# Optimization experiments

Hardware: AMD Instinct MI355X
Metric: run time of the kernel (lower is better)

## Reference

```python
import jax, jax.numpy as jnp
import numpy as np

B, S, D = 8, 1024, 512
H, Q, V = 8, 64, 64
NEG_INF = -2.0**32 + 1.0  # faithful to the TF module's mask fill value


def setup_inputs() -> dict:
    key = jax.random.key(0)
    ks = jax.random.split(key, 9)
    s = lambda fan_in: 1.0 / np.sqrt(fan_in)
    return {
        "x": jax.random.normal(ks[0], (B, S, D), dtype=jnp.float32),
        "Wq": jax.random.normal(ks[1], (D, Q * H), dtype=jnp.float32) * s(D),
        "bq": jnp.zeros((Q * H,), dtype=jnp.float32),
        "Wk": jax.random.normal(ks[2], (D, Q * H), dtype=jnp.float32) * s(D),
        "bk": jnp.zeros((Q * H,), dtype=jnp.float32),
        "Wv": jax.random.normal(ks[3], (D, V * H), dtype=jnp.float32) * s(D),
        "bv": jnp.zeros((V * H,), dtype=jnp.float32),
        "Wo": jax.random.normal(ks[4], (V * H, D), dtype=jnp.float32) * s(V * H),
        "bo": jnp.zeros((D,), dtype=jnp.float32),
    }


def _split_heads(t, hd):
    # [B,S,h*hd] -> split along last axis into h, concat along axis0 -> [h*B,S,hd]
    b, seq, _ = t.shape
    return t.reshape(b, seq, H, hd).transpose(2, 0, 1, 3).reshape(H * b, seq, hd)


def reference(x, Wq, bq, Wk, bk, Wv, bv, Wo, bo):
    q = _split_heads(x @ Wq + bq, Q)  # [h*B, S, q]
    k = _split_heads(x @ Wk + bk, Q)  # [h*B, S, q]
    v = _split_heads(x @ Wv + bv, V)  # [h*B, S, v]

    score = jnp.einsum("nsq,ntq->nst", q, k)  # [h*B, S, S], NOTE: no 1/sqrt(d) scaling (faithful)
    heatmap_score = score

    # stage == 'train': causal mask, masked entries set to -2^32 + 1
    mask = jnp.tril(jnp.ones((S, S), dtype=bool))
    score = jnp.where(mask, score, jnp.full_like(score, NEG_INF))
    attn = jax.nn.softmax(score, axis=-1)

    wv = jnp.einsum("nst,ntv->nsv", attn, v)  # [h*B, S, v]
    # split along axis0 into h, concat along last axis -> [B, S, h*v]
    wv = wv.reshape(H, B, S, V).transpose(1, 2, 0, 3).reshape(B, S, H * V)
    out = wv @ Wo + bo  # [B, S, D]
    return (out, heatmap_score)
```

## Files before the change

### kernel.cpp

```cpp
#include <hip/hip_runtime.h>


typedef unsigned short u16;
typedef unsigned int u32;
typedef __attribute__((ext_vector_type(8))) short bf8;
typedef __attribute__((ext_vector_type(4))) float f4;

__device__ __forceinline__ u16 f2bf(float f) {
    u32 x = __builtin_bit_cast(u32, f);
    return (u16)((x + 0x7FFFu + ((x >> 16) & 1u)) >> 16);
}

#define MFMA16(a, b, c) __builtin_amdgcn_mfma_f32_16x16x32_bf16((a), (b), (c), 0, 0, 0)

#define GLD16(gp, lp) __builtin_amdgcn_global_load_lds( \
    (const __attribute__((address_space(1))) unsigned int*)(gp), \
    (__attribute__((address_space(3))) unsigned int*)(lp), 16, 0, 0)

__global__ __launch_bounds__(256) void k_cvt_x(const float4* __restrict__ xi,
                                               ushort4* __restrict__ xo)
{
    int idx = blockIdx.x * 256 + threadIdx.x;
    for (int i = idx; i < 1048576; i += 262144) {
        float4 f = xi[i];
        ushort4 o;
        o.x = f2bf(f.x); o.y = f2bf(f.y); o.z = f2bf(f.z); o.w = f2bf(f.w);
        xo[i] = o;
    }
}

__global__ __launch_bounds__(256) void k_cvt_wT(
    const float* __restrict__ Wq, const float* __restrict__ Wk,
    const float* __restrict__ Wv, const float* __restrict__ Wo,
    u16* __restrict__ WqT, u16* __restrict__ WkT,
    u16* __restrict__ WvT, u16* __restrict__ WoT)
{
    const int z = blockIdx.z;
    const float* __restrict__ W = (z == 0) ? Wq : (z == 1) ? Wk : (z == 2) ? Wv : Wo;
    u16* __restrict__ WT        = (z == 0) ? WqT : (z == 1) ? WkT : (z == 2) ? WvT : WoT;

    __shared__ __align__(16) u16 Ts[64 * 72];
    const int k0 = blockIdx.x * 64, c0 = blockIdx.y * 64;
    const int tid = threadIdx.x;
    const int r = tid >> 4, cc = (tid & 15) * 4;
    #pragma unroll
    for (int rr = r; rr < 64; rr += 16) {
        float4 f = *(const float4*)&W[(size_t)(k0 + rr) * 512 + c0 + cc];
        Ts[(cc + 0) * 72 + rr] = f2bf(f.x);
        Ts[(cc + 1) * 72 + rr] = f2bf(f.y);
        Ts[(cc + 2) * 72 + rr] = f2bf(f.z);
        Ts[(cc + 3) * 72 + rr] = f2bf(f.w);
    }
    __syncthreads();
    #pragma unroll
    for (int i = 0; i < 2; ++i) {
        int gi = tid + i * 256;
        int cr = gi >> 3, g = gi & 7;
        bf8 v = *(bf8*)&Ts[cr * 72 + g * 8];
        *(bf8*)&WT[(size_t)(c0 + cr) * 512 + k0 + g * 8] = v;
    }
}

__global__ __launch_bounds__(256) void k_qkv(
    const u16* __restrict__ xb,
    const u16* __restrict__ WqT, const u16* __restrict__ WkT, const u16* __restrict__ WvT,
    const float* __restrict__ bq, const float* __restrict__ bk, const float* __restrict__ bv,
    u16* __restrict__ qb, u16* __restrict__ kb, u16* __restrict__ vT)
{
    const int which = blockIdx.z;
    const u16* __restrict__ WT     = (which == 0) ? WqT : (which == 1) ? WkT : WvT;
    const float* __restrict__ bias = (which == 0) ? bq : (which == 1) ? bk : bv;

    const int colTile = blockIdx.x * 128;
    const int rowTile = blockIdx.y * 128;

    __shared__ __align__(16) u16 As[128 * 64];
    __shared__ __align__(16) u16 Bs[128 * 64];

    const int tid = threadIdx.x;
    const int lane = tid & 63, w = tid >> 6;
    const int lm = lane & 15, kq = lane >> 4;
    const int mB = (w >> 1) * 64, nB = (w & 1) * 64;

    const int sr = lane >> 3;
    const int sg = (lane & 7) ^ sr;

    f4 acc[4][4] = {};

    for (int k0 = 0; k0 < 512; k0 += 64) {
        __syncthreads();
        #pragma unroll
        for (int i = 0; i < 4; ++i) {
            const int rb = w * 32 + i * 8;
            GLD16(&xb[(size_t)(rowTile + rb + sr) * 512 + k0 + sg * 8], &As[rb * 64]);
            GLD16(&WT[(size_t)(colTile + rb + sr) * 512 + k0 + sg * 8], &Bs[rb * 64]);
        }
        __syncthreads();
        #pragma unroll
        for (int ks = 0; ks < 2; ++ks) {
            bf8 a[4], b[4];
            #pragma unroll
            for (int mi = 0; mi < 4; ++mi)
                a[mi] = *(bf8*)&As[(mB + mi * 16 + lm) * 64 + (((ks * 4 + kq) ^ (lm & 7)) * 8)];
            #pragma unroll
            for (int ni = 0; ni < 4; ++ni)
                b[ni] = *(bf8*)&Bs[(nB + ni * 16 + lm) * 64 + (((ks * 4 + kq) ^ (lm & 7)) * 8)];
            #pragma unroll
            for (int mi = 0; mi < 4; ++mi)
                #pragma unroll
                for (int ni = 0; ni < 4; ++ni)
                    acc[mi][ni] = MFMA16(a[mi], b[ni], acc[mi][ni]);
        }
    }

    if (which < 2) {
        u16* __restrict__ outp = (which == 0) ? qb : kb;
        #pragma unroll
        for (int mi = 0; mi < 4; ++mi) {
            const int r0 = rowTile + mB + mi * 16 + kq * 4;
            #pragma unroll
            for (int ni = 0; ni < 4; ++ni) {
                const int c = colTile + nB + ni * 16 + lm;
                const float bv_ = bias[c];
                const int h = c >> 6, hd = c & 63;
                #pragma unroll
                for (int rg = 0; rg < 4; ++rg) {
                    const int rr = r0 + rg;
                    const int b = rr >> 10, s = rr & 1023;
                    outp[(size_t)(((h * 8 + b) << 10) + s) * 64 + hd] = f2bf(acc[mi][ni][rg] + bv_);
                }
            }
        }
    } else {
        #pragma unroll
        for (int mi = 0; mi < 4; ++mi) {
            const int r0 = rowTile + mB + mi * 16 + kq * 4;
            const int b = r0 >> 10, s0 = r0 & 1023;
            #pragma unroll
            for (int ni = 0; ni < 4; ++ni) {
                const int c = colTile + nB + ni * 16 + lm;
                const float bv_ = bias[c];
                const int h = c >> 6, hd = c & 63;
                ushort4 pk;
                pk.x = f2bf(acc[mi][ni][0] + bv_);
                pk.y = f2bf(acc[mi][ni][1] + bv_);
                pk.z = f2bf(acc[mi][ni][2] + bv_);
                pk.w = f2bf(acc[mi][ni][3] + bv_);
                *(ushort4*)&vT[(size_t)((h * 8 + b) * 64 + hd) * 1024 + s0] = pk;
            }
        }
    }
}

__global__ __launch_bounds__(256) void k_attn(
    const u16* __restrict__ qb, const u16* __restrict__ kb, const u16* __restrict__ vT,
    float* __restrict__ heat, u16* __restrict__ wvb)
{
    const int bid = blockIdx.x;
    const int sT = (bid < 256) ? (7 - (bid >> 6)) : ((bid >> 6) - 4);
    const int n = bid & 63;
    const int s0 = sT * 128;

    __shared__ __align__(16) u16 Kb[2][128 * 64];
    __shared__ __align__(16) u16 Vb[2][64 * 128];

    const int tid = threadIdx.x;
    const int lane = tid & 63, w = tid >> 6;
    const int lm = lane & 15, kq = lane >> 4;
    const int mB = w * 32;

    const int sr = lane >> 3, sg = (lane & 7) ^ sr;
    const int vr = lane >> 4, vg = lane & 15;

    const u16* __restrict__ qn = qb + (size_t)n * 65536;
    const u16* __restrict__ kn = kb + (size_t)n * 65536;
    const u16* __restrict__ vn = vT + (size_t)n * 65536;
    float* __restrict__ hp = heat + ((size_t)n << 20);

    #pragma unroll
    for (int i = 0; i < 4; ++i) {
        const int rb = w * 32 + i * 8;
        GLD16(&kn[(size_t)(rb + sr) * 64 + sg * 8], &Kb[0][rb * 64]);
    }
    #pragma unroll
    for (int i = 0; i < 4; ++i) {
        const int rb = w * 16 + i * 4;
        const int r = rb + vr;
        GLD16(&vn[(size_t)r * 1024 + ((vg ^ (r & 7)) * 8)], &Vb[0][rb * 128]);
    }

    bf8 aq[2][2];
    #pragma unroll
    for (int mi = 0; mi < 2; ++mi)
        #pragma unroll
        for (int ks = 0; ks < 2; ++ks)
            aq[mi][ks] = *(const bf8*)&qn[(size_t)(s0 + mB + mi * 16 + lm) * 64 + ks * 32 + kq * 8];

    f4 accO[2][4] = {};
    float m_i[2][4], l_i[2][4];
    #pragma unroll
    for (int mi = 0; mi < 2; ++mi)
        #pragma unroll
        for (int rg = 0; rg < 4; ++rg) { m_i[mi][rg] = -3.0e38f; l_i[mi][rg] = 0.f; }

    int c = 0;
    for (int tt = 0; tt < 8; ++tt, c ^= 1) {
        const int t0 = tt * 128;
        const bool causal = (tt <= sT);
        u16* __restrict__ Kc = &Kb[c][0];
        u16* __restrict__ Vc = &Vb[c][0];

        __syncthreads();

        if (tt < 7) {
            u16* __restrict__ Kn2 = &Kb[c ^ 1][0];
            #pragma unroll
            for (int i = 0; i < 4; ++i) {
                const int rb = w * 32 + i * 8;
                GLD16(&kn[(size_t)(t0 + 128 + rb + sr) * 64 + sg * 8], &Kn2[rb * 64]);
            }
            if (tt + 1 <= sT) {
                u16* __restrict__ Vn2 = &Vb[c ^ 1][0];
                #pragma unroll
                for (int i = 0; i < 4; ++i) {
                    const int rb = w * 16 + i * 4;
                    const int r = rb + vr;
                    GLD16(&vn[(size_t)r * 1024 + t0 + 128 + ((vg ^ (r & 7)) * 8)], &Vn2[rb * 128]);
                }
            }
        }

        f4 accS[2][8] = {};
        __builtin_amdgcn_s_setprio(1);
        #pragma unroll
        for (int ks = 0; ks < 2; ++ks) {
            bf8 b[8];
            #pragma unroll
            for (int ni = 0; ni < 8; ++ni)
                b[ni] = *(bf8*)&Kc[(ni * 16 + lm) * 64 + (((ks * 4 + kq) ^ (lm & 7)) * 8)];
            #pragma unroll
            for (int mi = 0; mi < 2; ++mi)
                #pragma unroll
                for (int ni = 0; ni < 8; ++ni)
                    accS[mi][ni] = MFMA16(aq[mi][ks], b[ni], accS[mi][ni]);
        }
        __builtin_amdgcn_s_setprio(0);

        #pragma unroll
        for (int mi = 0; mi < 2; ++mi) {
            #pragma unroll
            for (int rg = 0; rg < 4; ++rg) {
                float* rowp = &hp[(size_t)(s0 + mB + mi * 16 + kq * 4 + rg) * 1024 + t0 + lm];
                #pragma unroll
                for (int ni = 0; ni < 8; ++ni)
                    __builtin_nontemporal_store(accS[mi][ni][rg], &rowp[ni * 16]);
            }
        }

        if (causal) {
            asm volatile("s_waitcnt lgkmcnt(0)" ::: "memory");
            __builtin_amdgcn_s_barrier();
            __builtin_amdgcn_sched_barrier(0);

            const bool diag = (tt == sT);
            #pragma unroll
            for (int mi = 0; mi < 2; ++mi) {
                #pragma unroll
                for (int rg = 0; rg < 4; ++rg) {
                    const int srow = s0 + mB + mi * 16 + kq * 4 + rg;
                    float tm = -3.0e38f;
                    #pragma unroll
                    for (int ni = 0; ni < 8; ++ni) {
                        float sv = accS[mi][ni][rg];
                        if (diag && (t0 + ni * 16 + lm > srow)) sv = -3.0e38f;
                        tm = fmaxf(tm, sv);
                    }
                    tm = fmaxf(tm, __shfl_xor(tm, 1));
                    tm = fmaxf(tm, __shfl_xor(tm, 2));
                    tm = fmaxf(tm, __shfl_xor(tm, 4));
                    tm = fmaxf(tm, __shfl_xor(tm, 8));
                    const float mn = fmaxf(m_i[mi][rg], tm);
                    const float alpha = __expf(m_i[mi][rg] - mn);
                    float rs = 0.f;
                    #pragma unroll
                    for (int ni = 0; ni < 8; ++ni) {
                        float sv = accS[mi][ni][rg];
                        const bool ok = !diag || (t0 + ni * 16 + lm <= srow);
                        float p = ok ? __expf(sv - mn) : 0.f;
                        rs += p;
                        accS[mi][ni][rg] = p;
                    }
                    rs += __shfl_xor(rs, 1);
                    rs += __shfl_xor(rs, 2);
                    rs += __shfl_xor(rs, 4);
                    rs += __shfl_xor(rs, 8);
                    l_i[mi][rg] = l_i[mi][rg] * alpha + rs;
                    m_i[mi][rg] = mn;
                    #pragma unroll
                    for (int vni = 0; vni < 4; ++vni) accO[mi][vni][rg] *= alpha;
                }
            }

            #pragma unroll
            for (int half = 0; half < 2; ++half) {
                #pragma unroll
                for (int mi = 0; mi < 2; ++mi) {
                    #pragma unroll
                    for (int rg = 0; rg < 4; ++rg) {
                        const int prow = mB + mi * 16 + kq * 4 + rg;
                        #pragma unroll
                        for (int nl = 0; nl < 4; ++nl) {
                            const float p = accS[mi][half * 4 + nl][rg];
                            Kc[prow * 64 + (((nl * 2 + (lm >> 3)) ^ (prow & 7)) * 8) + (lm & 7)] = f2bf(p);
                        }
                    }
                }
                asm volatile("s_waitcnt lgkmcnt(0)" ::: "memory");
                __builtin_amdgcn_sched_barrier(0);

                __builtin_amdgcn_s_setprio(1);
                #pragma unroll
                for (int kl = 0; kl < 2; ++kl) {
                    const int ks = half * 2 + kl;
                    bf8 a[2], b[4];
                    #pragma unroll
                    for (int mi = 0; mi < 2; ++mi)
                        a[mi] = *(bf8*)&Kc[(mB + mi * 16 + lm) * 64 + (((kl * 4 + kq) ^ (lm & 7)) * 8)];
                    #pragma unroll
                    for (int vni = 0; vni < 4; ++vni)
                        b[vni] = *(bf8*)&Vc[(vni * 16 + lm) * 128 + (((ks * 4 + kq) ^ (lm & 7)) * 8)];
                    #pragma unroll
                    for (int mi = 0; mi < 2; ++mi)
                        #pragma unroll
                        for (int vni = 0; vni < 4; ++vni)
                            accO[mi][vni] = MFMA16(a[mi], b[vni], accO[mi][vni]);
                }
                __builtin_amdgcn_s_setprio(0);

                if (half == 0) {
                    asm volatile("s_waitcnt lgkmcnt(0)" ::: "memory");
                    __builtin_amdgcn_sched_barrier(0);
                }
            }
        }
    }

    u16* __restrict__ wn = wvb + (size_t)n * 65536;
    #pragma unroll
    for (int mi = 0; mi < 2; ++mi) {
        #pragma unroll
        for (int rg = 0; rg < 4; ++rg) {
            const float li = 1.0f / l_i[mi][rg];
            const int s = s0 + mB + mi * 16 + kq * 4 + rg;
            #pragma unroll
            for (int vni = 0; vni < 4; ++vni)
                wn[(size_t)s * 64 + vni * 16 + lm] = f2bf(accO[mi][vni][rg] * li);
        }
    }
}

__global__ __launch_bounds__(256) void k_out(
    const u16* __restrict__ wvb, const u16* __restrict__ WoT, const float* __restrict__ bo,
    float* __restrict__ outp)
{
    const int colTile = blockIdx.x * 128;
    const int rowTile = blockIdx.y * 128;
    const int b = rowTile >> 10, s0 = rowTile & 1023;

    __shared__ __align__(16) u16 As[128 * 64];
    __shared__ __align__(16) u16 Bs[128 * 64];

    const int tid = threadIdx.x;
    const int lane = tid & 63, w = tid >> 6;
    const int lm = lane & 15, kq = lane >> 4;
    const int mB = (w >> 1) * 64, nB = (w & 1) * 64;

    const int sr = lane >> 3;
    const int sg = (lane & 7) ^ sr;

    f4 acc[4][4] = {};

    for (int k0 = 0; k0 < 512; k0 += 64) {
        const int h = k0 >> 6;
        const u16* __restrict__ abase = wvb + (size_t)((h * 8 + b) * 1024 + s0) * 64;
        __syncthreads();
        #pragma unroll
        for (int i = 0; i < 4; ++i) {
            const int rb = w * 32 + i * 8;
            GLD16(&abase[(size_t)(rb + sr) * 64 + sg * 8], &As[rb * 64]);
            GLD16(&WoT[(size_t)(colTile + rb + sr) * 512 + k0 + sg * 8], &Bs[rb * 64]);
        }
        __syncthreads();
        #pragma unroll
        for (int ks = 0; ks < 2; ++ks) {
            bf8 a[4], b2[4];
            #pragma unroll
            for (int mi = 0; mi < 4; ++mi)
                a[mi] = *(bf8*)&As[(mB + mi * 16 + lm) * 64 + (((ks * 4 + kq) ^ (lm & 7)) * 8)];
            #pragma unroll
            for (int ni = 0; ni < 4; ++ni)
                b2[ni] = *(bf8*)&Bs[(nB + ni * 16 + lm) * 64 + (((ks * 4 + kq) ^ (lm & 7)) * 8)];
            #pragma unroll
            for (int mi = 0; mi < 4; ++mi)
                #pragma unroll
                for (int ni = 0; ni < 4; ++ni)
                    acc[mi][ni] = MFMA16(a[mi], b2[ni], acc[mi][ni]);
        }
    }

    #pragma unroll
    for (int mi = 0; mi < 4; ++mi) {
        const int r0 = rowTile + mB + mi * 16 + kq * 4;
        #pragma unroll
        for (int ni = 0; ni < 4; ++ni) {
            const int c = colTile + nB + ni * 16 + lm;
            const float bv_ = bo[c];
            #pragma unroll
            for (int rg = 0; rg < 4; ++rg)
                __builtin_nontemporal_store(acc[mi][ni][rg] + bv_,
                                            &outp[(size_t)(r0 + rg) * 512 + c]);
        }
    }
}

extern "C" void kernel_launch(void* const* d_in, const int* in_sizes, int n_in,
                              void* d_out, int out_size, void* d_ws, size_t ws_size,
                              hipStream_t stream)
{
    (void)in_sizes; (void)n_in; (void)out_size; (void)ws_size;

    const float* x  = (const float*)d_in[0];
    const float* Wq = (const float*)d_in[1];
    const float* bq = (const float*)d_in[2];
    const float* Wk = (const float*)d_in[3];
    const float* bk = (const float*)d_in[4];
    const float* Wv = (const float*)d_in[5];
    const float* bv = (const float*)d_in[6];
    const float* Wo = (const float*)d_in[7];
    const float* bo = (const float*)d_in[8];

    float* outp = (float*)d_out;
    float* heat = outp + 4194304;

    u16* ws16 = (u16*)d_ws;
    u16* xb  = ws16;
    u16* WqT = xb  + 4194304;
    u16* WkT = WqT + 262144;
    u16* WvT = WkT + 262144;
    u16* WoT = WvT + 262144;
    u16* qb  = WoT + 262144;
    u16* kb  = qb  + 4194304;
    u16* vT  = kb  + 4194304;
    u16* wvb = vT  + 4194304;

    k_cvt_x <<<1024, 256, 0, stream>>>((const float4*)x, (ushort4*)xb);
    k_cvt_wT<<<dim3(8, 8, 4), 256, 0, stream>>>(Wq, Wk, Wv, Wo, WqT, WkT, WvT, WoT);
    k_qkv   <<<dim3(4, 64, 3), 256, 0, stream>>>(xb, WqT, WkT, WvT, bq, bk, bv, qb, kb, vT);
    k_attn  <<<dim3(512), 256, 0, stream>>>(qb, kb, vT, heat, wvb);
    k_out   <<<dim3(4, 64), 256, 0, stream>>>(wvb, WoT, bo, outp);
}
```

Baseline: 389.1 us.

## Halve attention query tile to 64 rows, single-buffer V, remap blocks

Each attention block now handles 64 query rows (16 per wave) instead of 128, so the grid doubles to 1024 blocks with launch bounds requesting 3 blocks per SM. V is single-buffered and loaded within the current iteration, guarded by a vmcnt wait, which cuts LDS use. Block-to-head/row-tile mapping is reordered to interleave heads and balance causal work. The aim is more parallelism and occupancy for the heatmap-write-bound kernel, at the cost of reloading K for twice as many blocks and exposing V load latency.

```diff
diff --git a/kernel.cpp b/kernel.cpp
--- a/kernel.cpp
+++ b/kernel.cpp
@@ -152,22 +152,26 @@
     }
 }
 
-__global__ __launch_bounds__(256) void k_attn(
+__global__ __launch_bounds__(256, 3) void k_attn(
     const u16* __restrict__ qb, const u16* __restrict__ kb, const u16* __restrict__ vT,
     float* __restrict__ heat, u16* __restrict__ wvb)
 {
     const int bid = blockIdx.x;
-    const int sT = (bid < 256) ? (7 - (bid >> 6)) : ((bid >> 6) - 4);
-    const int n = bid & 63;
-    const int s0 = sT * 128;
+    const int p = bid >> 3;
+    const int n = (bid & 7) * 8 + (p & 7);
+    const int i4 = p >> 3;
+    const int q2 = i4 >> 2, j4 = i4 & 3;
+    const int rT = (q2 == 0) ? 15 - j4 : (q2 == 1) ? 8 + j4 : (q2 == 2) ? 7 - j4 : j4;
+    const int s0 = rT * 64;
+    const int sTT = rT >> 1;
 
     __shared__ __align__(16) u16 Kb[2][128 * 64];
-    __shared__ __align__(16) u16 Vb[2][64 * 128];
+    __shared__ __align__(16) u16 Vs[64 * 128];
 
     const int tid = threadIdx.x;
     const int lane = tid & 63, w = tid >> 6;
     const int lm = lane & 15, kq = lane >> 4;
-    const int mB = w * 32;
+    const int mB = w * 16;
 
     const int sr = lane >> 3, sg = (lane & 7) ^ sr;
     const int vr = lane >> 4, vg = lane & 15;
@@ -178,59 +182,47 @@
     float* __restrict__ hp = heat + ((size_t)n << 20);
 
     #pragma unroll
-    for (int i = 0; i < 4; ++i) {
-        const int rb = w * 32 + i * 8;
+    for (int ii = 0; ii < 4; ++ii) {
+        const int rb = w * 32 + ii * 8;
         GLD16(&kn[(size_t)(rb + sr) * 64 + sg * 8], &Kb[0][rb * 64]);
     }
-    #pragma unroll
-    for (int i = 0; i < 4; ++i) {
-        const int rb = w * 16 + i * 4;
-        const int r = rb + vr;
-        GLD16(&vn[(size_t)r * 1024 + ((vg ^ (r & 7)) * 8)], &Vb[0][rb * 128]);
-    }
-
-    bf8 aq[2][2];
-    #pragma unroll
-    for (int mi = 0; mi < 2; ++mi)
-        #pragma unroll
-        for (int ks = 0; ks < 2; ++ks)
-            aq[mi][ks] = *(const bf8*)&qn[(size_t)(s0 + mB + mi * 16 + lm) * 64 + ks * 32 + kq * 8];
-
-    f4 accO[2][4] = {};
-    float m_i[2][4], l_i[2][4];
-    #pragma unroll
-    for (int mi = 0; mi < 2; ++mi)
-        #pragma unroll
-        for (int rg = 0; rg < 4; ++rg) { m_i[mi][rg] = -3.0e38f; l_i[mi][rg] = 0.f; }
+
+    bf8 aq[2];
+    #pragma unroll
+    for (int ks = 0; ks < 2; ++ks)
+        aq[ks] = *(const bf8*)&qn[(size_t)(s0 + mB + lm) * 64 + ks * 32 + kq * 8];
+
+    f4 accO[4] = {};
+    float m_i[4], l_i[4];
+    #pragma unroll
+    for (int rg = 0; rg < 4; ++rg) { m_i[rg] = -3.0e38f; l_i[rg] = 0.f; }
 
     int c = 0;
     for (int tt = 0; tt < 8; ++tt, c ^= 1) {
         const int t0 = tt * 128;
-        const bool causal = (tt <= sT);
+        const bool causal = (tt <= sTT);
         u16* __restrict__ Kc = &Kb[c][0];
-        u16* __restrict__ Vc = &Vb[c][0];
 
         __syncthreads();
 
+        if (causal) {
+            #pragma unroll
+            for (int ii = 0; ii < 4; ++ii) {
+                const int rb = w * 16 + ii * 4;
+                const int r = rb + vr;
+                GLD16(&vn[(size_t)r * 1024 + t0 + ((vg ^ (r & 7)) * 8)], &Vs[rb * 128]);
+            }
+        }
         if (tt < 7) {
             u16* __restrict__ Kn2 = &Kb[c ^ 1][0];
             #pragma unroll
-            for (int i = 0; i < 4; ++i) {
-                const int rb = w * 32 + i * 8;
+            for (int ii = 0; ii < 4; ++ii) {
+                const int rb = w * 32 + ii * 8;
                 GLD16(&kn[(size_t)(t0 + 128 + rb + sr) * 64 + sg * 8], &Kn2[rb * 64]);
             }
-            if (tt + 1 <= sT) {
-                u16* __restrict__ Vn2 = &Vb[c ^ 1][0];
-                #pragma unroll
-                for (int i = 0; i < 4; ++i) {
-                    const int rb = w * 16 + i * 4;
-                    const int r = rb + vr;
-                    GLD16(&vn[(size_t)r * 1024 + t0 + 128 + ((vg ^ (r & 7)) * 8)], &Vn2[rb * 128]);
-                }
-            }
-        }
-
-        f4 accS[2][8] = {};
+        }
+
+        f4 accS[8] = {};
         __builtin_amdgcn_s_setprio(1);
         #pragma unroll
         for (int ks = 0; ks < 2; ++ks) {
@@ -239,80 +231,69 @@
             for (int ni = 0; ni < 8; ++ni)
                 b[ni] = *(bf8*)&Kc[(ni * 16 + lm) * 64 + (((ks * 4 + kq) ^ (lm & 7)) * 8)];
             #pragma unroll
-            for (int mi = 0; mi < 2; ++mi)
-                #pragma unroll
-                for (int ni = 0; ni < 8; ++ni)
-                    accS[mi][ni] = MFMA16(aq[mi][ks], b[ni], accS[mi][ni]);
+            for (int ni = 0; ni < 8; ++ni)
+                accS[ni] = MFMA16(aq[ks], b[ni], accS[ni]);
         }
         __builtin_amdgcn_s_setprio(0);
 
         #pragma unroll
-        for (int mi = 0; mi < 2; ++mi) {
-            #pragma unroll
-            for (int rg = 0; rg < 4; ++rg) {
-                float* rowp = &hp[(size_t)(s0 + mB + mi * 16 + kq * 4 + rg) * 1024 + t0 + lm];
-                #pragma unroll
-                for (int ni = 0; ni < 8; ++ni)
-                    __builtin_nontemporal_store(accS[mi][ni][rg], &rowp[ni * 16]);
-            }
+        for (int rg = 0; rg < 4; ++rg) {
+            float* rowp = &hp[(size_t)(s0 + mB + kq * 4 + rg) * 1024 + t0 + lm];
+            #pragma unroll
+            for (int ni = 0; ni < 8; ++ni)
+                __builtin_nontemporal_store(accS[ni][rg], &rowp[ni * 16]);
         }
 
         if (causal) {
-            asm volatile("s_waitcnt lgkmcnt(0)" ::: "memory");
+            asm volatile("s_waitcnt vmcnt(0) lgkmcnt(0)" ::: "memory");
             __builtin_amdgcn_s_barrier();
             __builtin_amdgcn_sched_barrier(0);
 
-            const bool diag = (tt == sT);
-            #pragma unroll
-            for (int mi = 0; mi < 2; ++mi) {
+            const bool diag = (tt == sTT);
+            #pragma unroll
+            for (int rg = 0; rg < 4; ++rg) {
+                const int srow = s0 + mB + kq * 4 + rg;
+                float tm = -3.0e38f;
+                #pragma unroll
+                for (int ni = 0; ni < 8; ++ni) {
+                    float sv = accS[ni][rg];
+                    if (diag && (t0 + ni * 16 + lm > srow)) sv = -3.0e38f;
+                    tm = fmaxf(tm, sv);
+                }
+                tm = fmaxf(tm, __shfl_xor(tm, 1));
+                tm = fmaxf(tm, __shfl_xor(tm, 2));
+                tm = fmaxf(tm, __shfl_xor(tm, 4));
+                tm = fmaxf(tm, __shfl_xor(tm, 8));
+                const float mn = fmaxf(m_i[rg], tm);
+                const float alpha = __expf(m_i[rg] - mn);
+                float rs = 0.f;
+                #pragma unroll
+                for (int ni = 0; ni < 8; ++ni) {
+                    float sv = accS[ni][rg];
+                    const bool ok = !diag || (t0 + ni * 16 + lm <= srow);
+                    float pv = ok ? __expf(sv - mn) : 0.f;
+                    rs += pv;
+                    accS[ni][rg] = pv;
+                }
+                rs += __shfl_xor(rs, 1);
+                rs += __shfl_xor(rs, 2);
+                rs += __shfl_xor(rs, 4);
+                rs += __shfl_xor(rs, 8);
+                l_i[rg] = l_i[rg] * alpha + rs;
+                m_i[rg] = mn;
+                #pragma unroll
+                for (int vni = 0; vni < 4; ++vni) accO[vni][rg] *= alpha;
+            }
+
+            #pragma unroll
+            for (int half = 0; half < 2; ++half) {
                 #pragma unroll
                 for (int rg = 0; rg < 4; ++rg) {
-                    const int srow = s0 + mB + mi * 16 + kq * 4 + rg;
-                    float tm = -3.0e38f;
+                    const int prow = mB + kq * 4 + rg;
                     #pragma unroll
-                    for (int ni = 0; ni < 8; ++ni) {
-                        float sv = accS[mi][ni][rg];
-                        if (diag && (t0 + ni * 16 + lm > srow)) sv = -3.0e38f;
-                        tm = fmaxf(tm, sv);
-                    }
-                    tm = fmaxf(tm, __shfl_xor(tm, 1));
-                    tm = fmaxf(tm, __shfl_xor(tm, 2));
-                    tm = fmaxf(tm, __shfl_xor(tm, 4));
-                    tm = fmaxf(tm, __shfl_xor(tm, 8));
-                    const float mn = fmaxf(m_i[mi][rg], tm);
-                    const float alpha = __expf(m_i[mi][rg] - mn);
-                    float rs = 0.f;
-                    #pragma unroll
-                    for (int ni = 0; ni < 8; ++ni) {
-                        float sv = accS[mi][ni][rg];
-                        const bool ok = !diag || (t0 + ni * 16 + lm <= srow);
-                        float p = ok ? __expf(sv - mn) : 0.f;
-                        rs += p;
-                        accS[mi][ni][rg] = p;
-                    }
-                    rs += __shfl_xor(rs, 1);
-                    rs += __shfl_xor(rs, 2);
-                    rs += __shfl_xor(rs, 4);
-                    rs += __shfl_xor(rs, 8);
-                    l_i[mi][rg] = l_i[mi][rg] * alpha + rs;
-                    m_i[mi][rg] = mn;
-                    #pragma unroll
-                    for (int vni = 0; vni < 4; ++vni) accO[mi][vni][rg] *= alpha;
-                }
-            }
-
-            #pragma unroll
-            for (int half = 0; half < 2; ++half) {
-                #pragma unroll
-                for (int mi = 0; mi < 2; ++mi) {
-                    #pragma unroll
-                    for (int rg = 0; rg < 4; ++rg) {
-                        const int prow = mB + mi * 16 + kq * 4 + rg;
-                        #pragma unroll
-                        for (int nl = 0; nl < 4; ++nl) {
-                            const float p = accS[mi][half * 4 + nl][rg];
-                            Kc[prow * 64 + (((nl * 2 + (lm >> 3)) ^ (prow & 7)) * 8) + (lm & 7)] = f2bf(p);
-                        }
+                    for (int nl = 0; nl < 4; ++nl) {
+                        const float pv = accS[half * 4 + nl][rg];
+                        Kc[prow * 64 + (((nl * 2 + (lm >> 3)) ^ (prow & 7)) * 8) + (lm & 7)] = f2bf(pv);
                     }
                 }
                 asm volatile("s_waitcnt lgkmcnt(0)" ::: "memory");
@@ -322,18 +303,14 @@
                 #pragma unroll
                 for (int kl = 0; kl < 2; ++kl) {
                     const int ks = half * 2 + kl;
-                    bf8 a[2], b[4];
-                    #pragma unroll
-                    for (int mi = 0; mi < 2; ++mi)
-                        a[mi] = *(bf8*)&Kc[(mB + mi * 16 + lm) * 64 + (((kl * 4 + kq) ^ (lm & 7)) * 8)];
+                    bf8 a, b[4];
+                    a = *(bf8*)&Kc[(mB + lm) * 64 + (((kl * 4 + kq) ^ (lm & 7)) * 8)];
                     #pragma unroll
                     for (int vni = 0; vni < 4; ++vni)
-                        b[vni] = *(bf8*)&Vc[(vni * 16 + lm) * 128 + (((ks * 4 + kq) ^ (lm & 7)) * 8)];
+                        b[vni] = *(bf8*)&Vs[(vni * 16 + lm) * 128 + (((ks * 4 + kq) ^ (lm & 7)) * 8)];
                     #pragma unroll
-                    for (int mi = 0; mi < 2; ++mi)
-                        #pragma unroll
-                        for (int vni = 0; vni < 4; ++vni)
-                            accO[mi][vni] = MFMA16(a[mi], b[vni], accO[mi][vni]);
+                    for (int vni = 0; vni < 4; ++vni)
+                        accO[vni] = MFMA16(a, b[vni], accO[vni]);
                 }
                 __builtin_amdgcn_s_setprio(0);
 
@@ -347,15 +324,12 @@
 
     u16* __restrict__ wn = wvb + (size_t)n * 65536;
     #pragma unroll
-    for (int mi = 0; mi < 2; ++mi) {
-        #pragma unroll
-        for (int rg = 0; rg < 4; ++rg) {
-            const float li = 1.0f / l_i[mi][rg];
-            const int s = s0 + mB + mi * 16 + kq * 4 + rg;
-            #pragma unroll
-            for (int vni = 0; vni < 4; ++vni)
-                wn[(size_t)s * 64 + vni * 16 + lm] = f2bf(accO[mi][vni][rg] * li);
-        }
+    for (int rg = 0; rg < 4; ++rg) {
+        const float li = 1.0f / l_i[rg];
+        const int s = s0 + mB + kq * 4 + rg;
+        #pragma unroll
+        for (int vni = 0; vni < 4; ++vni)
+            wn[(size_t)s * 64 + vni * 16 + lm] = f2bf(accO[vni][rg] * li);
     }
 }
 
@@ -456,6 +430,6 @@
     k_cvt_x <<<1024, 256, 0, stream>>>((const float4*)x, (ushort4*)xb);
     k_cvt_wT<<<dim3(8, 8, 4), 256, 0, stream>>>(Wq, Wk, Wv, Wo, WqT, WkT, WvT, WoT);
     k_qkv   <<<dim3(4, 64, 3), 256, 0, stream>>>(xb, WqT, WkT, WvT, bq, bk, bv, qb, kb, vT);
-    k_attn  <<<dim3(512), 256, 0, stream>>>(qb, kb, vT, heat, wvb);
+    k_attn  <<<dim3(1024), 256, 0, stream>>>(qb, kb, vT, heat, wvb);
     k_out   <<<dim3(4, 64), 256, 0, stream>>>(wvb, WoT, bo, outp);
 }
```

After: 380.0 us. 1.02x faster.
